# Kernel tuning notes

Hardware: AMD Instinct MI355X
Metric: run time of the kernel (lower is better)

The kernel has to match this reference:

```python
import jax, jax.numpy as jnp
import numpy as np

B, S, D, H = 2, 2048, 1024, 16
DK = D // H
NEG = -1.0e9


def setup_inputs() -> dict:
    key = jax.random.key(0)
    ks = jax.random.split(key, 11)
    inp = {
        "q": jax.random.normal(ks[0], (B, S, D), jnp.float32),
        "k": jax.random.normal(ks[1], (B, S, D), jnp.float32),
        "v": jax.random.normal(ks[2], (B, S, D), jnp.float32),
        "mask": jnp.tril(jnp.ones((S, S), jnp.int32))[None, None],  # causal [1,1,S,S]
    }
    scale = 0.02
    inp["w_q"] = jax.random.normal(ks[3], (D, D), jnp.float32) * scale
    inp["b_q"] = jnp.zeros((D,), jnp.float32)
    inp["w_k"] = jax.random.normal(ks[4], (D, D), jnp.float32) * scale
    inp["b_k"] = jnp.zeros((D,), jnp.float32)
    inp["w_v"] = jax.random.normal(ks[5], (D, D), jnp.float32) * scale
    inp["b_v"] = jnp.zeros((D,), jnp.float32)
    inp["w_o"] = jax.random.normal(ks[6], (D, D), jnp.float32) * scale
    inp["b_o"] = jnp.zeros((D,), jnp.float32)
    return inp


def reference(q, k, v, mask, w_q, b_q, w_k, b_k, w_v, b_v, w_o, b_o):
    # projections: [B,S,D] -> [B,H,S,DK]
    def proj(x, w, b):
        y = jnp.einsum("bsd,de->bse", x, w) + b
        return y.reshape(B, S, H, DK).transpose(0, 2, 1, 3)

    Q = proj(q, w_q, b_q)
    K = proj(k, w_k, b_k)
    V = proj(v, w_v, b_v)
    # explicit scores matrix, faithful to the original naive attention
    scores = jnp.einsum("bhsd,bhtd->bhst", Q, K) / jnp.sqrt(jnp.float32(DK))
    scores = jnp.where(mask == 0, NEG, scores)
    attn = jax.nn.softmax(scores, axis=-1)  # dropout p=0.0 -> identity
    x = jnp.einsum("bhst,bhtd->bhsd", attn, V)
    x = x.transpose(0, 2, 1, 3).reshape(B, S, D)
    return jnp.einsum("bsd,de->bse", x, w_o) + b_o
```

## Files before the change

kernel.cpp:

```cpp
#include <hip/hip_runtime.h>
#include <hip/hip_bf16.h>

typedef __bf16 bf16;
typedef __bf16 bf16x2 __attribute__((ext_vector_type(2)));
typedef __bf16 bf16x8 __attribute__((ext_vector_type(8)));
typedef float f32x4 __attribute__((ext_vector_type(4)));

#define MFMA16(a, b, c) __builtin_amdgcn_mfma_f32_16x16x32_bf16(a, b, c, 0, 0, 0)

#define QSCALE 0.18033688f

#define GLOAD_LDS(g, l)                                              \
  __builtin_amdgcn_global_load_lds(                                  \
      (const __attribute__((address_space(1))) void*)(g),            \
      (__attribute__((address_space(3))) void*)(l), 16, 0, 0)

__global__ __launch_bounds__(256) void convert_k(const float* __restrict__ q,
                                                 const float* __restrict__ k,
                                                 const float* __restrict__ v,
                                                 bf16* __restrict__ qb,
                                                 bf16* __restrict__ kb,
                                                 bf16* __restrict__ vb) {
  const float* src = blockIdx.y == 0 ? q : blockIdx.y == 1 ? k : v;
  bf16* dst = blockIdx.y == 0 ? qb : blockIdx.y == 1 ? kb : vb;
  const size_t i = ((size_t)blockIdx.x * 256 + threadIdx.x) * 8;
  float4 a = *(const float4*)(src + i);
  float4 b = *(const float4*)(src + i + 4);
  bf16x8 o;
  o[0] = (bf16)a.x; o[1] = (bf16)a.y; o[2] = (bf16)a.z; o[3] = (bf16)a.w;
  o[4] = (bf16)b.x; o[5] = (bf16)b.y; o[6] = (bf16)b.z; o[7] = (bf16)b.w;
  *(bf16x8*)(dst + i) = o;
}

__global__ __launch_bounds__(256) void transpose_w(const float* __restrict__ w0,
                                                   const float* __restrict__ w1,
                                                   const float* __restrict__ w2,
                                                   const float* __restrict__ w3,
                                                   bf16* __restrict__ dst) {
  __shared__ bf16 T[64][68];
  const float* W = blockIdx.z == 0 ? w0 : blockIdx.z == 1 ? w1
                   : blockIdx.z == 2 ? w2 : w3;
  bf16* Y = dst + (size_t)blockIdx.z * 1024 * 1024;
  const int t = threadIdx.x, r = t >> 2, c4 = t & 3;
  const int k0 = blockIdx.y * 64, n0 = blockIdx.x * 64;

  const float4* src = (const float4*)(W + (size_t)(k0 + r) * 1024 + n0 + c4 * 16);
  float4 f0 = src[0], f1 = src[1], f2 = src[2], f3 = src[3];
  bf16* row = &T[r][c4 * 16];
  row[0] = (bf16)f0.x; row[1] = (bf16)f0.y; row[2] = (bf16)f0.z; row[3] = (bf16)f0.w;
  row[4] = (bf16)f1.x; row[5] = (bf16)f1.y; row[6] = (bf16)f1.z; row[7] = (bf16)f1.w;
  row[8] = (bf16)f2.x; row[9] = (bf16)f2.y; row[10] = (bf16)f2.z; row[11] = (bf16)f2.w;
  row[12] = (bf16)f3.x; row[13] = (bf16)f3.y; row[14] = (bf16)f3.z; row[15] = (bf16)f3.w;
  __syncthreads();

  bf16x8 o0, o1;
#pragma unroll
  for (int j = 0; j < 8; ++j) o0[j] = T[c4 * 16 + j][r];
#pragma unroll
  for (int j = 0; j < 8; ++j) o1[j] = T[c4 * 16 + 8 + j][r];
  bf16* d = Y + (size_t)(n0 + r) * 1024 + k0 + c4 * 16;
  *(bf16x8*)d = o0;
  *(bf16x8*)(d + 8) = o1;
}

template <int MODE>
__global__ __launch_bounds__(256) void gemm_k(const bf16* __restrict__ X,
                                              const bf16* __restrict__ Bt,
                                              const float* __restrict__ bias,
                                              void* __restrict__ Yv,
                                              float escale) {
  __shared__ bf16 Al[128 * 32];
  __shared__ bf16 Bl[64 * 32];

  const int t = threadIdx.x;
  const int wave = t >> 6, lane = t & 63, quad = lane >> 4, l16 = lane & 15;
  const int wm = (wave >> 1) * 64, wn = (wave & 1) * 32;
  const int bm = blockIdx.y * 128, bn = blockIdx.x * 64;

  const int off = wave * 1024 + lane * 16;
  const int srow = off >> 6;
  const int scol = (off & 63) >> 1;
  const bf16* gA0 = X + (size_t)(bm + srow) * 1024 + scol;
  const bf16* gA1 = X + (size_t)(bm + 64 + srow) * 1024 + scol;
  const bf16* gB = Bt + (size_t)(bn + srow) * 1024 + scol;
  bf16* ldsA0 = Al + wave * 512;
  bf16* ldsA1 = Al + 2048 + wave * 512;
  bf16* ldsB = Bl + wave * 512;

  f32x4 acc[4][2] = {};

  for (int kb = 0; kb < 1024; kb += 32) {
    GLOAD_LDS(gA0 + kb, ldsA0);
    GLOAD_LDS(gA1 + kb, ldsA1);
    GLOAD_LDS(gB + kb, ldsB);
    __syncthreads();

    bf16x8 af[4], bfr[2];
#pragma unroll
    for (int mt = 0; mt < 4; ++mt)
      af[mt] = *(const bf16x8*)(Al + (wm + mt * 16 + l16) * 32 + quad * 8);
#pragma unroll
    for (int nt = 0; nt < 2; ++nt)
      bfr[nt] = *(const bf16x8*)(Bl + (wn + nt * 16 + l16) * 32 + quad * 8);
#pragma unroll
    for (int mt = 0; mt < 4; ++mt)
#pragma unroll
      for (int nt = 0; nt < 2; ++nt)
        acc[mt][nt] = MFMA16(af[mt], bfr[nt], acc[mt][nt]);
    __syncthreads();
  }

#pragma unroll
  for (int mt = 0; mt < 4; ++mt)
#pragma unroll
    for (int nt = 0; nt < 2; ++nt) {
      const int gn = bn + wn + nt * 16 + l16;
      const float bia = bias[gn];
#pragma unroll
      for (int r = 0; r < 4; ++r) {
        const int gm = bm + wm + mt * 16 + quad * 4 + r;
        const float val = (acc[mt][nt][r] + bia) * escale;
        if (MODE == 0) {
          ((float*)Yv)[(size_t)gm * 1024 + gn] = val;
        } else {
          const int b = gm >> 11, s = gm & 2047;
          const int h = gn >> 6, dk = gn & 63;
          size_t addr;
          if (MODE == 1)
            addr = ((size_t)(b * 16 + h) * 2048 + s) * 64 + dk;
          else
            addr = ((size_t)(b * 16 + h) * 64 + dk) * 2048 + s;
          ((bf16*)Yv)[addr] = (bf16)val;
        }
      }
    }
}

__global__ __launch_bounds__(256) void attn_k(const bf16* __restrict__ Q,
                                              const bf16* __restrict__ K,
                                              const bf16* __restrict__ Vt,
                                              bf16* __restrict__ X) {
  __shared__ bf16 Kl[64 * 72];
  __shared__ bf16 Vl[64 * 72];
  __shared__ bf16 Pb[4][16 * 72];

  const int t = threadIdx.x;
  const int wave = t >> 6, lane = t & 63, quad = lane >> 4, l16 = lane & 15;
  const int pairx = blockIdx.x, bh = blockIdx.y;
  const int b = bh >> 4, h = bh & 15;

  const bf16* Qb = Q + (size_t)bh * 2048 * 64;
  const bf16* Kb = K + (size_t)bh * 2048 * 64;
  const bf16* Vb = Vt + (size_t)bh * 64 * 2048;

  const int srow = t >> 2;
  const int scol = (t & 3) * 16;

  bf16x8 onesf;
#pragma unroll
  for (int i = 0; i < 8; ++i) onesf[i] = (bf16)1.0f;

  bf16* Pw = Pb[wave];

  for (int phase = 0; phase < 2; ++phase) {
    const int qtile = phase ? (31 - pairx) : pairx;
    const int ntiles = qtile + 1;
    const int q0 = qtile * 64 + wave * 16;

    bf16x8 qf0 = *(const bf16x8*)(Qb + (q0 + l16) * 64 + quad * 8);
    bf16x8 qf1 = *(const bf16x8*)(Qb + (q0 + l16) * 64 + 32 + quad * 8);

    f32x4 o[4] = {};
    f32x4 o4 = {};

    {
      const bf16* kp = Kb + srow * 64 + scol;
      const bf16* vp = Vb + (size_t)srow * 2048 + scol;
      bf16x8 k0r = *(const bf16x8*)kp;
      bf16x8 k1r = *(const bf16x8*)(kp + 8);
      bf16x8 v0r = *(const bf16x8*)vp;
      bf16x8 v1r = *(const bf16x8*)(vp + 8);
      *(bf16x8*)(Kl + srow * 72 + scol) = k0r;
      *(bf16x8*)(Kl + srow * 72 + scol + 8) = k1r;
      *(bf16x8*)(Vl + srow * 72 + scol) = v0r;
      *(bf16x8*)(Vl + srow * 72 + scol + 8) = v1r;
    }
    __syncthreads();

    for (int kt = 0; kt < ntiles; ++kt) {
      const int k0 = kt * 64;
      const bool more = (kt + 1) < ntiles;
      bf16x8 kr0, kr1, vr0, vr1;
      if (more) {
        const bf16* kp = Kb + (k0 + 64 + srow) * 64 + scol;
        const bf16* vp = Vb + (size_t)srow * 2048 + k0 + 64 + scol;
        kr0 = *(const bf16x8*)kp;
        kr1 = *(const bf16x8*)(kp + 8);
        vr0 = *(const bf16x8*)vp;
        vr1 = *(const bf16x8*)(vp + 8);
      }

      f32x4 sc[4];
#pragma unroll
      for (int nt = 0; nt < 4; ++nt) {
        bf16x8 kf0 = *(const bf16x8*)(Kl + (nt * 16 + l16) * 72 + quad * 8);
        bf16x8 kf1 = *(const bf16x8*)(Kl + (nt * 16 + l16) * 72 + 32 + quad * 8);
        f32x4 s = {};
        s = MFMA16(qf0, kf0, s);
        s = MFMA16(qf1, kf1, s);
        sc[nt] = s;
      }

#pragma unroll
      for (int r = 0; r < 4; ++r) {
        const int row = quad * 4 + r;
        const int qg = q0 + row;
#pragma unroll
        for (int nt = 0; nt < 4; ++nt) {
          const int key = k0 + nt * 16 + l16;
          const float p = (key <= qg) ? exp2f(sc[nt][r]) : 0.f;
          Pw[row * 72 + nt * 16 + l16] = (bf16)p;
        }
      }
      __builtin_amdgcn_s_waitcnt(0xC07F);

      bf16x8 pf0 = *(const bf16x8*)(Pw + l16 * 72 + quad * 8);
      bf16x8 pf1 = *(const bf16x8*)(Pw + l16 * 72 + 32 + quad * 8);
      o4 = MFMA16(pf0, onesf, o4);
      o4 = MFMA16(pf1, onesf, o4);
#pragma unroll
      for (int dt = 0; dt < 4; ++dt) {
        bf16x8 vf0 = *(const bf16x8*)(Vl + (dt * 16 + l16) * 72 + quad * 8);
        bf16x8 vf1 = *(const bf16x8*)(Vl + (dt * 16 + l16) * 72 + 32 + quad * 8);
        o[dt] = MFMA16(pf0, vf0, o[dt]);
        o[dt] = MFMA16(pf1, vf1, o[dt]);
      }

      __syncthreads();
      if (more) {
        *(bf16x8*)(Kl + srow * 72 + scol) = kr0;
        *(bf16x8*)(Kl + srow * 72 + scol + 8) = kr1;
        *(bf16x8*)(Vl + srow * 72 + scol) = vr0;
        *(bf16x8*)(Vl + srow * 72 + scol + 8) = vr1;
        __syncthreads();
      }
    }

#pragma unroll
    for (int r = 0; r < 4; ++r) {
      const float rinv = 1.0f / o4[r];
      const int qg = q0 + quad * 4 + r;
#pragma unroll
      for (int dt = 0; dt < 4; ++dt) {
        const int col = h * 64 + dt * 16 + l16;
        X[((size_t)b * 2048 + qg) * 1024 + col] = (bf16)(o[dt][r] * rinv);
      }
    }
    __syncthreads();
  }
}

extern "C" void kernel_launch(void* const* d_in, const int* in_sizes, int n_in,
                              void* d_out, int out_size, void* d_ws,
                              size_t ws_size, hipStream_t stream) {
  const float* q = (const float*)d_in[0];
  const float* k = (const float*)d_in[1];
  const float* v = (const float*)d_in[2];
  const float* w_q = (const float*)d_in[4];
  const float* b_q = (const float*)d_in[5];
  const float* w_k = (const float*)d_in[6];
  const float* b_k = (const float*)d_in[7];
  const float* w_v = (const float*)d_in[8];
  const float* b_v = (const float*)d_in[9];
  const float* w_o = (const float*)d_in[10];
  const float* b_o = (const float*)d_in[11];

  bf16* ws = (bf16*)d_ws;
  const size_t NELEM = (size_t)4096 * 1024;
  bf16* Qp = ws;
  bf16* Kp = ws + NELEM;
  bf16* Vtp = ws + 2 * NELEM;
  bf16* Xp = ws + 3 * NELEM;
  bf16* Wt = ws + 4 * NELEM;
  bf16* Wtq = Wt, *Wtk = Wt + 1048576, *Wtv = Wt + 2097152, *Wto = Wt + 3145728;
  bf16* qb = Xp;
  bf16* kb = (bf16*)d_out;
  bf16* vb = kb + NELEM;

  convert_k<<<dim3(2048, 3), 256, 0, stream>>>(q, k, v, qb, kb, vb);
  transpose_w<<<dim3(16, 16, 4), 256, 0, stream>>>(w_q, w_k, w_v, w_o, Wt);

  dim3 gg(16, 32), bb(256);
  gemm_k<1><<<gg, bb, 0, stream>>>(qb, Wtq, b_q, Qp, QSCALE);
  gemm_k<1><<<gg, bb, 0, stream>>>(kb, Wtk, b_k, Kp, 1.0f);
  gemm_k<2><<<gg, bb, 0, stream>>>(vb, Wtv, b_v, Vtp, 1.0f);
  attn_k<<<dim3(16, 32), bb, 0, stream>>>(Qp, Kp, Vtp, Xp);
  gemm_k<0><<<gg, bb, 0, stream>>>(Xp, Wto, b_o, (float*)d_out, 1.0f);
}
```

Measured before the change: 269.7 us.

## Merge QKV projections into one launch and widen GEMM tiles to 128x128

The three separate Q/K/V projection GEMM launches become a single launch that uses blockIdx.z to pick the input, weight, bias and output layout. The GEMM tile widens from 128x64 to 128x128, so each wave computes a 64x64 sub-tile with 16 accumulators and A-tile loads are reused across twice as many columns. This cuts launch overhead and global/LDS traffic per FLOP. The cost is more registers per thread and fewer blocks (256 per projection), which may lower occupancy on the 256-CU device.

```diff
diff --git a/kernel.cpp b/kernel.cpp
--- a/kernel.cpp
+++ b/kernel.cpp
@@ -63,49 +63,59 @@
   *(bf16x8*)(d + 8) = o1;
 }
 
-template <int MODE>
-__global__ __launch_bounds__(256) void gemm_k(const bf16* __restrict__ X,
-                                              const bf16* __restrict__ Bt,
-                                              const float* __restrict__ bias,
-                                              void* __restrict__ Yv,
-                                              float escale) {
+template <int QKV>
+__global__ __launch_bounds__(256) void gemm128(
+    const bf16* __restrict__ xq, const bf16* __restrict__ xk,
+    const bf16* __restrict__ xv, const bf16* __restrict__ Wt,
+    const float* __restrict__ bq, const float* __restrict__ bk,
+    const float* __restrict__ bv, bf16* __restrict__ Qp,
+    bf16* __restrict__ Kp, bf16* __restrict__ Vtp, float* __restrict__ Yf) {
   __shared__ bf16 Al[128 * 32];
-  __shared__ bf16 Bl[64 * 32];
+  __shared__ bf16 Bl[128 * 32];
+
+  const int z = QKV ? blockIdx.z : 0;
+  const bf16* X = QKV ? (z == 0 ? xq : z == 1 ? xk : xv) : xq;
+  const bf16* Bt = Wt + (size_t)z * 1048576;
+  const float* bias = QKV ? (z == 0 ? bq : z == 1 ? bk : bv) : bq;
+  const float escale = (QKV && z == 0) ? QSCALE : 1.0f;
 
   const int t = threadIdx.x;
   const int wave = t >> 6, lane = t & 63, quad = lane >> 4, l16 = lane & 15;
-  const int wm = (wave >> 1) * 64, wn = (wave & 1) * 32;
-  const int bm = blockIdx.y * 128, bn = blockIdx.x * 64;
+  const int wm = (wave >> 1) * 64, wn = (wave & 1) * 64;
+  const int bm = blockIdx.y * 128, bn = blockIdx.x * 128;
 
   const int off = wave * 1024 + lane * 16;
   const int srow = off >> 6;
   const int scol = (off & 63) >> 1;
   const bf16* gA0 = X + (size_t)(bm + srow) * 1024 + scol;
   const bf16* gA1 = X + (size_t)(bm + 64 + srow) * 1024 + scol;
-  const bf16* gB = Bt + (size_t)(bn + srow) * 1024 + scol;
+  const bf16* gB0 = Bt + (size_t)(bn + srow) * 1024 + scol;
+  const bf16* gB1 = Bt + (size_t)(bn + 64 + srow) * 1024 + scol;
   bf16* ldsA0 = Al + wave * 512;
   bf16* ldsA1 = Al + 2048 + wave * 512;
-  bf16* ldsB = Bl + wave * 512;
-
-  f32x4 acc[4][2] = {};
+  bf16* ldsB0 = Bl + wave * 512;
+  bf16* ldsB1 = Bl + 2048 + wave * 512;
+
+  f32x4 acc[4][4] = {};
 
   for (int kb = 0; kb < 1024; kb += 32) {
     GLOAD_LDS(gA0 + kb, ldsA0);
     GLOAD_LDS(gA1 + kb, ldsA1);
-    GLOAD_LDS(gB + kb, ldsB);
+    GLOAD_LDS(gB0 + kb, ldsB0);
+    GLOAD_LDS(gB1 + kb, ldsB1);
     __syncthreads();
 
-    bf16x8 af[4], bfr[2];
+    bf16x8 af[4], bfr[4];
 #pragma unroll
     for (int mt = 0; mt < 4; ++mt)
       af[mt] = *(const bf16x8*)(Al + (wm + mt * 16 + l16) * 32 + quad * 8);
 #pragma unroll
-    for (int nt = 0; nt < 2; ++nt)
+    for (int nt = 0; nt < 4; ++nt)
       bfr[nt] = *(const bf16x8*)(Bl + (wn + nt * 16 + l16) * 32 + quad * 8);
 #pragma unroll
     for (int mt = 0; mt < 4; ++mt)
 #pragma unroll
-      for (int nt = 0; nt < 2; ++nt)
+      for (int nt = 0; nt < 4; ++nt)
         acc[mt][nt] = MFMA16(af[mt], bfr[nt], acc[mt][nt]);
     __syncthreads();
   }
@@ -113,24 +123,24 @@
 #pragma unroll
   for (int mt = 0; mt < 4; ++mt)
 #pragma unroll
-    for (int nt = 0; nt < 2; ++nt) {
+    for (int nt = 0; nt < 4; ++nt) {
       const int gn = bn + wn + nt * 16 + l16;
       const float bia = bias[gn];
 #pragma unroll
       for (int r = 0; r < 4; ++r) {
         const int gm = bm + wm + mt * 16 + quad * 4 + r;
         const float val = (acc[mt][nt][r] + bia) * escale;
-        if (MODE == 0) {
-          ((float*)Yv)[(size_t)gm * 1024 + gn] = val;
+        if (!QKV) {
+          Yf[(size_t)gm * 1024 + gn] = val;
         } else {
           const int b = gm >> 11, s = gm & 2047;
           const int h = gn >> 6, dk = gn & 63;
-          size_t addr;
-          if (MODE == 1)
-            addr = ((size_t)(b * 16 + h) * 2048 + s) * 64 + dk;
-          else
-            addr = ((size_t)(b * 16 + h) * 64 + dk) * 2048 + s;
-          ((bf16*)Yv)[addr] = (bf16)val;
+          if (z <= 1) {
+            bf16* Y = (z == 0) ? Qp : Kp;
+            Y[((size_t)(b * 16 + h) * 2048 + s) * 64 + dk] = (bf16)val;
+          } else {
+            Vtp[((size_t)(b * 16 + h) * 64 + dk) * 2048 + s] = (bf16)val;
+          }
         }
       }
     }
@@ -282,7 +292,7 @@
   bf16* Vtp = ws + 2 * NELEM;
   bf16* Xp = ws + 3 * NELEM;
   bf16* Wt = ws + 4 * NELEM;
-  bf16* Wtq = Wt, *Wtk = Wt + 1048576, *Wtv = Wt + 2097152, *Wto = Wt + 3145728;
+  bf16* Wto = Wt + 3145728;
   bf16* qb = Xp;
   bf16* kb = (bf16*)d_out;
   bf16* vb = kb + NELEM;
@@ -290,10 +300,10 @@
   convert_k<<<dim3(2048, 3), 256, 0, stream>>>(q, k, v, qb, kb, vb);
   transpose_w<<<dim3(16, 16, 4), 256, 0, stream>>>(w_q, w_k, w_v, w_o, Wt);
 
-  dim3 gg(16, 32), bb(256);
-  gemm_k<1><<<gg, bb, 0, stream>>>(qb, Wtq, b_q, Qp, QSCALE);
-  gemm_k<1><<<gg, bb, 0, stream>>>(kb, Wtk, b_k, Kp, 1.0f);
-  gemm_k<2><<<gg, bb, 0, stream>>>(vb, Wtv, b_v, Vtp, 1.0f);
-  attn_k<<<dim3(16, 32), bb, 0, stream>>>(Qp, Kp, Vtp, Xp);
-  gemm_k<0><<<gg, bb, 0, stream>>>(Xp, Wto, b_o, (float*)d_out, 1.0f);
-}
+  gemm128<1><<<dim3(8, 32, 3), 256, 0, stream>>>(qb, kb, vb, Wt, b_q, b_k, b_v,
+                                                 Qp, Kp, Vtp, nullptr);
+  attn_k<<<dim3(16, 32), 256, 0, stream>>>(Qp, Kp, Vtp, Xp);
+  gemm128<0><<<dim3(8, 32), 256, 0, stream>>>(Xp, nullptr, nullptr, Wto, b_o,
+                                              nullptr, nullptr, nullptr,
+                                              nullptr, nullptr, (float*)d_out);
+}
```

Result: faster. 256.4 us (-4.9%).
